# Performance work log

Hardware: AMD Instinct MI355X
Metric: run time of the kernel (lower is better)

## Reference

```python
import jax, jax.numpy as jnp
import numpy as np

H_NODE = 256
H_EDGE = 64
B = 8        # number of graphs
A_PER = 64   # anchors per graph
N_PER = 512  # nodes per graph
INF = 1000000.0
EPS = 1e-8
D_MIN, D_MAX = 0.0, 20.0  # _rbf defaults (gvp-style)


def setup_inputs() -> dict:
    key = jax.random.key(0)
    ks = jax.random.split(key, 16)
    h, he = H_NODE, H_EDGE
    n = lambda k, shp, s=1.0: jax.random.normal(k, shp, jnp.float32) * s
    return {
        "anchor_x": n(ks[0], (B * A_PER, 3), 10.0),
        "node_x": n(ks[1], (B * N_PER, 3), 10.0),
        "anchor_features": n(ks[2], (B * A_PER, h)),
        "node_features": n(ks[3], (B * N_PER, h)),
        "batch": jnp.repeat(jnp.arange(B, dtype=jnp.int32), N_PER),
        "anchor_batch": jnp.repeat(jnp.arange(B, dtype=jnp.int32), A_PER),
        "node_mask": (jax.random.uniform(ks[4], (B * N_PER,)) < 0.9).astype(jnp.float32),
        "Wq": n(ks[5], (h, h), h ** -0.5), "bq": jnp.zeros((h,), jnp.float32),
        "Wkv": n(ks[6], (2 * h, h + he), (h + he) ** -0.5), "bkv": jnp.zeros((2 * h,), jnp.float32),
        "ln1_g": jnp.ones((h,), jnp.float32), "ln1_b": jnp.zeros((h,), jnp.float32),
        "W1": n(ks[7], (2 * h, h), h ** -0.5), "b1": jnp.zeros((2 * h,), jnp.float32),
        "W2": n(ks[8], (2 * h, 2 * h), (2 * h) ** -0.5), "b2": jnp.zeros((2 * h,), jnp.float32),
        "W3": n(ks[9], (h, 2 * h), (2 * h) ** -0.5), "b3": jnp.zeros((h,), jnp.float32),
        "ln2_g": jnp.ones((h,), jnp.float32), "ln2_b": jnp.zeros((h,), jnp.float32),
    }


def _ln(x, g, b, eps=1e-5):
    m = x.mean(-1, keepdims=True)
    v = ((x - m) ** 2).mean(-1, keepdims=True)
    return (x - m) * jax.lax.rsqrt(v + eps) * g + b


def _forward(anchor_x, node_x, anchor_features, node_features, node_mask,
             Wq, bq, Wkv, bkv, ln1_g, ln1_b, W1, b1, W2, b2, W3, b3, ln2_g, ln2_b):
    h, he = H_NODE, H_EDGE
    # equal-sized graphs: reshape global tensors to [B, ., .] (batch ids are repeat(arange(B)))
    q = (anchor_features @ Wq.T + bq).reshape(B, A_PER, h)
    ax = anchor_x.reshape(B, A_PER, 3)
    nx = node_x.reshape(B, N_PER, 3)
    nf = node_features.reshape(B, N_PER, h)
    mask = node_mask.reshape(B, N_PER)

    # pairwise anchor->node distances; original adds scalar eps to the diff vector before the norm
    dist = jnp.linalg.norm(ax[:, :, None, :] - nx[:, None, :, :] + EPS, axis=-1)  # [B,A,N]

    # RBF featurization of dist/10 with D_count = h_edge
    mu = jnp.linspace(D_MIN, D_MAX, he)
    sigma = (D_MAX - D_MIN) / he
    rbf = jnp.exp(-(((dist / 10.0)[..., None] - mu) / sigma) ** 2)  # [B,A,N,he]

    # kv_node(cat([node_feat, rbf])) decomposed: node part computed once per node
    Wkv_n, Wkv_e = Wkv[:, :h], Wkv[:, h:]
    kv_n = nf @ Wkv_n.T + bkv                 # [B,N,2h]
    kv_e = rbf @ Wkv_e.T                      # [B,A,N,2h]
    kv = kv_n[:, None, :, :] + kv_e           # [B,A,N,2h]
    k, v = kv[..., :h], kv[..., h:]

    attn = jnp.einsum('bah,banh->ban', q, k)
    attn = attn * ((mask[:, None, :] - 1.0) * INF)  # faithful to original (multiplicative mask)
    attn = jax.nn.softmax(attn, axis=-1)
    upd = jnp.einsum('ban,banh->bah', attn, v).reshape(B * A_PER, h)

    af = _ln(anchor_features + upd, ln1_g, ln1_b)
    m = jax.nn.relu(af @ W1.T + b1)
    m = jax.nn.relu(m @ W2.T + b2)
    m = m @ W3.T + b3
    return _ln(af + m, ln2_g, ln2_b)


def reference(anchor_x, node_x, anchor_features, node_features, batch, anchor_batch, node_mask,
              Wq, bq, Wkv, bkv, ln1_g, ln1_b, W1, b1, W2, b2, W3, b3, ln2_g, ln2_b):
    # batch / anchor_batch encode equal-sized contiguous graphs; structure is baked into reshapes
    return _forward(anchor_x, node_x, anchor_features, node_features, node_mask,
                    Wq, bq, Wkv, bkv, ln1_g, ln1_b, W1, b1, W2, b2, W3, b3, ln2_g, ln2_b)
```

## Files before the change

kernel.cpp:

```cpp
#include <hip/hip_runtime.h>

#define H    256
#define HE   64
#define NPB  512
#define MU_STEP (20.0f / 63.0f)
#define INV_SIG 3.2f

__device__ __forceinline__ float wave_sum(float v) {
#pragma unroll
    for (int o = 32; o; o >>= 1) v += __shfl_xor(v, o, 64);
    return v;
}
__device__ __forceinline__ float wave_max(float v) {
#pragma unroll
    for (int o = 32; o; o >>= 1) v = fmaxf(v, __shfl_xor(v, o, 64));
    return v;
}
__device__ __forceinline__ float dot4(float4 a, float4 b, float acc) {
    return fmaf(a.x, b.x, fmaf(a.y, b.y, fmaf(a.z, b.z, fmaf(a.w, b.w, acc))));
}
__device__ __forceinline__ float4 add4(float4 a, float4 b) {
    return make_float4(a.x + b.x, a.y + b.y, a.z + b.z, a.w + b.w);
}

__global__ void __launch_bounds__(1024, 4) fused_all(
    const float* __restrict__ anchor_x, const float* __restrict__ node_x,
    const float* __restrict__ anchor_f, const float* __restrict__ node_f,
    const float* __restrict__ node_mask,
    const float* __restrict__ Wq,  const float* __restrict__ bq,
    const float* __restrict__ Wkv, const float* __restrict__ bkv,
    const float* __restrict__ ln1_g, const float* __restrict__ ln1_b,
    const float* __restrict__ W1, const float* __restrict__ b1,
    const float* __restrict__ W2, const float* __restrict__ b2,
    const float* __restrict__ W3, const float* __restrict__ b3,
    const float* __restrict__ g2,  const float* __restrict__ bb2,
    float* __restrict__ out)
{
    const int bid = blockIdx.x;
    const int b  = bid & 7;
    const int pr = bid >> 3;
    const int aA = b * 64 + 2 * pr;
    const int aB = aA + 1;
    const int t  = threadIdx.x;
    const int wv = t >> 6, l = t & 63;
    const int sub = l >> 4, kc16 = l & 15;

    __shared__ __align__(16) float qWp_s[2][2][324];
    __shared__ __align__(16) float q_s[2][256];
    __shared__ __align__(16) float af_s[2][256];
    __shared__ __align__(16) float d10_s[2][NPB];
    __shared__ __align__(16) float mf_s[NPB];
    __shared__ __align__(16) float lg_s[2][NPB];
    __shared__ __align__(16) float w_s[2][NPB];
    __shared__ __align__(16) float snf_s[2][256], rj_s[2][64];
    __shared__ __align__(16) float m1_s[2][512], m2_s[2][512];
    __shared__ __align__(16) float red[512], red16[32];
    __shared__ int   idx_s[2][NPB];
    __shared__ int   cnt_s[2];

    if (t < 128) {
        int hh = t >> 6, tt = t & 63;
        ((float4*)af_s[hh])[tt] =
            ((const float4*)anchor_f)[(size_t)(hh ? aB : aA) * 64 + tt];
    }
    if (t < 2) cnt_s[t] = 0;

    if (t < 512) {
        float axA0 = anchor_x[3 * aA], axA1 = anchor_x[3 * aA + 1], axA2 = anchor_x[3 * aA + 2];
        float axB0 = anchor_x[3 * aB], axB1 = anchor_x[3 * aB + 1], axB2 = anchor_x[3 * aB + 2];
        int ng = b * NPB + t;
        float nx0 = node_x[3 * ng], nx1 = node_x[3 * ng + 1], nx2 = node_x[3 * ng + 2];
        float dx = axA0 - nx0 + 1e-8f, dy = axA1 - nx1 + 1e-8f, dz = axA2 - nx2 + 1e-8f;
        d10_s[0][t] = sqrtf(dx * dx + dy * dy + dz * dz) * 0.1f;
        dx = axB0 - nx0 + 1e-8f; dy = axB1 - nx1 + 1e-8f; dz = axB2 - nx2 + 1e-8f;
        d10_s[1][t] = sqrtf(dx * dx + dy * dy + dz * dz) * 0.1f;
        mf_s[t] = (node_mask[ng] - 1.0f) * 1000000.0f;
    }
    __syncthreads();

    {
        float4 aA4[4], aB4[4];
#pragma unroll
        for (int v = 0; v < 4; ++v) {
            aA4[v] = ((const float4*)af_s[0])[16 * v + kc16];
            aB4[v] = ((const float4*)af_s[1])[16 * v + kc16];
        }
#pragma unroll
        for (int sp = 0; sp < 2; ++sp) {
            const int m0 = sp * 128 + wv * 4 + sub;
            const int m1 = m0 + 64;
            const float4* wr0 = (const float4*)(Wq + (size_t)m0 * 256);
            const float4* wr1 = (const float4*)(Wq + (size_t)m1 * 256);
            float4 w[8];
#pragma unroll
            for (int v = 0; v < 4; ++v) { w[v] = wr0[16 * v + kc16]; w[4 + v] = wr1[16 * v + kc16]; }
            float a0A = 0.f, a0B = 0.f, a1A = 0.f, a1B = 0.f;
#pragma unroll
            for (int v = 0; v < 4; ++v) {
                a0A = dot4(w[v],     aA4[v], a0A);
                a0B = dot4(w[v],     aB4[v], a0B);
                a1A = dot4(w[4 + v], aA4[v], a1A);
                a1B = dot4(w[4 + v], aB4[v], a1B);
            }
#pragma unroll
            for (int o = 8; o >= 1; o >>= 1) {
                a0A += __shfl_xor(a0A, o, 64);
                a0B += __shfl_xor(a0B, o, 64);
                a1A += __shfl_xor(a1A, o, 64);
                a1B += __shfl_xor(a1B, o, 64);
            }
            if (kc16 == 0) {
                q_s[0][m0] = a0A + bq[m0];
                q_s[1][m0] = a0B + bq[m0];
                q_s[0][m1] = a1A + bq[m1];
                q_s[1][m1] = a1B + bq[m1];
            }
        }
    }
    __syncthreads();

    {
        int grp = -1, col = 0;
        if (t < 320)                   { grp = 0; col = t; }
        else if (t >= 512 && t < 832)  { grp = 1; col = t - 512; }
        if (grp >= 0) {
            const int r0 = grp * 128;
            const float* qsA = q_s[0] + r0;
            const float* qsB = q_s[1] + r0;
            float accA = 0.f, accB = 0.f;
            for (int o = 0; o < 128; o += 16) {
                float w16[16];
#pragma unroll
                for (int u = 0; u < 16; ++u) w16[u] = Wkv[(size_t)(r0 + o + u) * 320 + col];
#pragma unroll
                for (int u = 0; u < 16; ++u) {
                    accA = fmaf(w16[u], qsA[o + u], accA);
                    accB = fmaf(w16[u], qsB[o + u], accB);
                }
            }
            qWp_s[grp][0][col] = accA;
            qWp_s[grp][1][col] = accB;
        }
    }
    {
        float p = (t < 512) ? q_s[t >> 8][t & 255] * bkv[t & 255] : 0.f;
        p = wave_sum(p);
        if (l == 0) red16[wv] = p;
    }
    __syncthreads();
    const float qbkA = red16[0] + red16[1] + red16[2] + red16[3];
    const float qbkB = red16[4] + red16[5] + red16[6] + red16[7];

    {
        const int g = sub;
        float4 qA4[4], qB4[4];
#pragma unroll
        for (int v = 0; v < 4; ++v) {
            qA4[v] = add4(((const float4*)qWp_s[0][0])[4 * kc16 + v],
                          ((const float4*)qWp_s[1][0])[4 * kc16 + v]);
            qB4[v] = add4(((const float4*)qWp_s[0][1])[4 * kc16 + v],
                          ((const float4*)qWp_s[1][1])[4 * kc16 + v]);
        }
        const float4 qeA4 = add4(((const float4*)(qWp_s[0][0] + 256))[kc16],
                                 ((const float4*)(qWp_s[1][0] + 256))[kc16]);
        const float4 qeB4 = add4(((const float4*)(qWp_s[0][1] + 256))[kc16],
                                 ((const float4*)(qWp_s[1][1] + 256))[kc16]);
        const float mu0 = (4 * kc16 + 0) * MU_STEP, mu1 = (4 * kc16 + 1) * MU_STEP;
        const float mu2 = (4 * kc16 + 2) * MU_STEP, mu3 = (4 * kc16 + 3) * MU_STEP;
        const float4* nfb = (const float4*)(node_f + (size_t)(b * NPB) * 256);

        float4 f[4], fn[4];
        {
            const size_t r0 = (size_t)(wv * 4 + g) * 64 + 4 * kc16;
#pragma unroll
            for (int v = 0; v < 4; ++v) f[v] = nfb[r0 + v];
        }
        for (int it = 0; it < 8; ++it) {
            const int n = it * 64 + wv * 4 + g;
            if (it < 7) {
                const size_t r1 = (size_t)(n + 64) * 64 + 4 * kc16;
#pragma unroll
                for (int v = 0; v < 4; ++v) fn[v] = nfb[r1 + v];
            }
            float sA = 0.f, sB = 0.f;
#pragma unroll
            for (int v = 0; v < 4; ++v) {
                sA = dot4(f[v], qA4[v], sA);
                sB = dot4(f[v], qB4[v], sB);
            }
            const float dA10 = d10_s[0][n], dB10 = d10_s[1][n];
            float u;
            u = (dA10 - mu0) * INV_SIG; sA = fmaf(qeA4.x, __expf(-u * u), sA);
            u = (dA10 - mu1) * INV_SIG; sA = fmaf(qeA4.y, __expf(-u * u), sA);
            u = (dA10 - mu2) * INV_SIG; sA = fmaf(qeA4.z, __expf(-u * u), sA);
            u = (dA10 - mu3) * INV_SIG; sA = fmaf(qeA4.w, __expf(-u * u), sA);
            u = (dB10 - mu0) * INV_SIG; sB = fmaf(qeB4.x, __expf(-u * u), sB);
            u = (dB10 - mu1) * INV_SIG; sB = fmaf(qeB4.y, __expf(-u * u), sB);
            u = (dB10 - mu2) * INV_SIG; sB = fmaf(qeB4.z, __expf(-u * u), sB);
            u = (dB10 - mu3) * INV_SIG; sB = fmaf(qeB4.w, __expf(-u * u), sB);
#pragma unroll
            for (int o = 8; o >= 1; o >>= 1) {
                sA += __shfl_xor(sA, o, 64);
                sB += __shfl_xor(sB, o, 64);
            }
            if (kc16 == 0) {
                lg_s[0][n] = (sA + qbkA) * mf_s[n];
                lg_s[1][n] = (sB + qbkB) * mf_s[n];
            }
#pragma unroll
            for (int v = 0; v < 4; ++v) f[v] = fn[v];
        }
    }
    __syncthreads();

    const int h8 = t >> 9, n9 = t & 511;
    float lg = lg_s[h8][n9];
    {
        float m = wave_max(lg);
        if (l == 0) red16[wv] = m;
    }
    __syncthreads();
    float gmA = red16[0], gmB = red16[8];
#pragma unroll
    for (int i = 1; i < 8; ++i) { gmA = fmaxf(gmA, red16[i]); gmB = fmaxf(gmB, red16[8 + i]); }
    float e = __expf(lg - (h8 ? gmB : gmA));
    w_s[h8][n9] = e;
    {
        float sm = wave_sum(e);
        if (l == 0) red16[16 + wv] = sm;
    }
    if (e > 0.f) { int p = atomicAdd(&cnt_s[h8], 1); idx_s[h8][p] = n9; }
    __syncthreads();
    float smA = 0.f, smB = 0.f;
#pragma unroll
    for (int i = 0; i < 8; ++i) { smA += red16[16 + i]; smB += red16[24 + i]; }
    const float invA = 1.0f / smA, invB = 1.0f / smB;

    if (t < 512) {
        const int hh = t >> 8, col = t & 255;
        const int cnt = cnt_s[hh];
        const float* base = node_f + (size_t)(b * NPB) * 256 + col;
        const int*   idx  = idx_s[hh];
        const float* ws   = w_s[hh];
        float s = 0.f;
        int i = 0;
        for (; i + 16 <= cnt; i += 16) {
            int   n[16];
            float f[16];
#pragma unroll
            for (int u = 0; u < 16; ++u) n[u] = idx[i + u];
#pragma unroll
            for (int u = 0; u < 16; ++u) f[u] = base[(size_t)n[u] * 256];
#pragma unroll
            for (int u = 0; u < 16; ++u) s = fmaf(ws[n[u]], f[u], s);
        }
        for (; i < cnt; ++i) { int n = idx[i]; s = fmaf(ws[n], base[(size_t)n * 256], s); }
        snf_s[hh][col] = s;
    } else {
        const int tt = t - 512;
        const int ha = tt >> 8, j = tt & 63, g = (tt >> 6) & 3;
        const int cnt = cnt_s[ha];
        const int*   idx = idx_s[ha];
        const float* ws  = w_s[ha];
        const float* ds  = d10_s[ha];
        const float mu = j * MU_STEP;
        float r = 0.f;
        int i = g;
        for (; i + 12 < cnt; i += 16) {
            int n0 = idx[i], n1 = idx[i + 4], n2 = idx[i + 8], n3 = idx[i + 12];
            float u0 = (ds[n0] - mu) * INV_SIG, u1 = (ds[n1] - mu) * INV_SIG;
            float u2 = (ds[n2] - mu) * INV_SIG, u3 = (ds[n3] - mu) * INV_SIG;
            r = fmaf(ws[n0], __expf(-u0 * u0), r);
            r = fmaf(ws[n1], __expf(-u1 * u1), r);
            r = fmaf(ws[n2], __expf(-u2 * u2), r);
            r = fmaf(ws[n3], __expf(-u3 * u3), r);
        }
        for (; i < cnt; i += 4) {
            int n = idx[i];
            float uu = (ds[n] - mu) * INV_SIG;
            r = fmaf(ws[n], __expf(-uu * uu), r);
        }
        red[tt] = r;
    }
    __syncthreads();
    if (t < 128) {
        int ha = t >> 6, j = t & 63;
        rj_s[ha][j] = red[ha * 256 + j] + red[ha * 256 + 64 + j]
                    + red[ha * 256 + 128 + j] + red[ha * 256 + 192 + j];
    }
    __syncthreads();

    {
        float4 sA4[4], sB4[4];
#pragma unroll
        for (int v = 0; v < 4; ++v) {
            sA4[v] = ((const float4*)snf_s[0])[16 * v + kc16];
            sB4[v] = ((const float4*)snf_s[1])[16 * v + kc16];
        }
        const float4 rA4 = ((const float4*)rj_s[0])[kc16];
        const float4 rB4 = ((const float4*)rj_s[1])[kc16];
#pragma unroll
        for (int pass = 0; pass < 4; ++pass) {
            int m = pass * 64 + wv * 4 + sub;
            const float4* wr = (const float4*)(Wkv + (size_t)(256 + m) * 320);
            float4 w[4];
#pragma unroll
            for (int v = 0; v < 4; ++v) w[v] = wr[16 * v + kc16];
            float4 w4 = wr[64 + kc16];
            float aAc = 0.f, aBc = 0.f;
#pragma unroll
            for (int v = 0; v < 4; ++v) {
                aAc = dot4(w[v], sA4[v], aAc);
                aBc = dot4(w[v], sB4[v], aBc);
            }
            aAc = dot4(w4, rA4, aAc);
            aBc = dot4(w4, rB4, aBc);
#pragma unroll
            for (int o = 8; o >= 1; o >>= 1) {
                aAc += __shfl_xor(aAc, o, 64);
                aBc += __shfl_xor(aBc, o, 64);
            }
            if (kc16 == 0) { red[m] = aAc; red[256 + m] = aBc; }
        }
    }
    __syncthreads();

    const int h = (t >> 8) & 1, th = t & 255;
    float x = 0.f;
    if (t < 512)
        x = af_s[h][th] + red[h * 256 + th] * (h ? invB : invA) + bkv[256 + th];
    {
        float s1 = wave_sum(x);
        float s2 = wave_sum(x * x);
        if (l == 0) { red16[wv] = s1; red16[16 + wv] = s2; }
    }
    __syncthreads();
    {
        float meanA = (red16[0] + red16[1] + red16[2] + red16[3]) * (1.0f / 256.0f);
        float meanB = (red16[4] + red16[5] + red16[6] + red16[7]) * (1.0f / 256.0f);
        float sqA   = (red16[16] + red16[17] + red16[18] + red16[19]) * (1.0f / 256.0f);
        float sqB   = (red16[20] + red16[21] + red16[22] + red16[23]) * (1.0f / 256.0f);
        float varA = sqA - meanA * meanA, varB = sqB - meanB * meanB;
        if (t < 512) {
            float xc = x - (h ? meanB : meanA);
            af_s[h][th] = xc * rsqrtf((h ? varB : varA) + 1e-5f) * ln1_g[th] + ln1_b[th];
        }
    }
    __syncthreads();

    {
        float4 aA4[4], aB4[4];
#pragma unroll
        for (int v = 0; v < 4; ++v) {
            aA4[v] = ((const float4*)af_s[0])[16 * v + kc16];
            aB4[v] = ((const float4*)af_s[1])[16 * v + kc16];
        }
#pragma unroll
        for (int sp = 0; sp < 4; ++sp) {
            const int m0 = sp * 128 + wv * 4 + sub;
            const int m1 = m0 + 64;
            const float4* wr0 = (const float4*)(W1 + (size_t)m0 * 256);
            const float4* wr1 = (const float4*)(W1 + (size_t)m1 * 256);
            float4 w[8];
#pragma unroll
            for (int v = 0; v < 4; ++v) { w[v] = wr0[16 * v + kc16]; w[4 + v] = wr1[16 * v + kc16]; }
            float a0A = 0.f, a0B = 0.f, a1A = 0.f, a1B = 0.f;
#pragma unroll
            for (int v = 0; v < 4; ++v) {
                a0A = dot4(w[v],     aA4[v], a0A);
                a0B = dot4(w[v],     aB4[v], a0B);
                a1A = dot4(w[4 + v], aA4[v], a1A);
                a1B = dot4(w[4 + v], aB4[v], a1B);
            }
#pragma unroll
            for (int o = 8; o >= 1; o >>= 1) {
                a0A += __shfl_xor(a0A, o, 64);
                a0B += __shfl_xor(a0B, o, 64);
                a1A += __shfl_xor(a1A, o, 64);
                a1B += __shfl_xor(a1B, o, 64);
            }
            if (kc16 == 0) {
                m1_s[0][m0] = fmaxf(a0A + b1[m0], 0.f);
                m1_s[1][m0] = fmaxf(a0B + b1[m0], 0.f);
                m1_s[0][m1] = fmaxf(a1A + b1[m1], 0.f);
                m1_s[1][m1] = fmaxf(a1B + b1[m1], 0.f);
            }
        }
    }
    __syncthreads();

#pragma unroll
    for (int pass = 0; pass < 8; ++pass) {
        int m = pass * 64 + wv * 4 + sub;
        const float4* wr = (const float4*)(W2 + (size_t)m * 512);
        float4 w[8];
#pragma unroll
        for (int k = 0; k < 8; ++k) w[k] = wr[k * 16 + kc16];
        const float4* mA = (const float4*)m1_s[0];
        const float4* mB = (const float4*)m1_s[1];
        float aAc = 0.f, aBc = 0.f;
#pragma unroll
        for (int k = 0; k < 8; ++k) {
            aAc = dot4(w[k], mA[k * 16 + kc16], aAc);
            aBc = dot4(w[k], mB[k * 16 + kc16], aBc);
        }
#pragma unroll
        for (int o = 8; o >= 1; o >>= 1) {
            aAc += __shfl_xor(aAc, o, 64);
            aBc += __shfl_xor(aBc, o, 64);
        }
        if (kc16 == 0) {
            float bv = b2[m];
            m2_s[0][m] = fmaxf(aAc + bv, 0.f);
            m2_s[1][m] = fmaxf(aBc + bv, 0.f);
        }
    }
    __syncthreads();

#pragma unroll
    for (int pass = 0; pass < 4; ++pass) {
        int m = pass * 64 + wv * 4 + sub;
        const float4* wr = (const float4*)(W3 + (size_t)m * 512);
        float4 w[8];
#pragma unroll
        for (int k = 0; k < 8; ++k) w[k] = wr[k * 16 + kc16];
        const float4* mA = (const float4*)m2_s[0];
        const float4* mB = (const float4*)m2_s[1];
        float aAc = 0.f, aBc = 0.f;
#pragma unroll
        for (int k = 0; k < 8; ++k) {
            aAc = dot4(w[k], mA[k * 16 + kc16], aAc);
            aBc = dot4(w[k], mB[k * 16 + kc16], aBc);
        }
#pragma unroll
        for (int o = 8; o >= 1; o >>= 1) {
            aAc += __shfl_xor(aAc, o, 64);
            aBc += __shfl_xor(aBc, o, 64);
        }
        if (kc16 == 0) {
            float bv = b3[m];
            red[m]       = aAc + bv;
            red[256 + m] = aBc + bv;
        }
    }
    __syncthreads();

    float y = 0.f;
    if (t < 512) y = red[h * 256 + th] + af_s[h][th];
    {
        float s1 = wave_sum(y);
        float s2 = wave_sum(y * y);
        if (l == 0) { red16[wv] = s1; red16[16 + wv] = s2; }
    }
    __syncthreads();
    {
        float mnA = (red16[0] + red16[1] + red16[2] + red16[3]) * (1.0f / 256.0f);
        float mnB = (red16[4] + red16[5] + red16[6] + red16[7]) * (1.0f / 256.0f);
        float sqA = (red16[16] + red16[17] + red16[18] + red16[19]) * (1.0f / 256.0f);
        float sqB = (red16[20] + red16[21] + red16[22] + red16[23]) * (1.0f / 256.0f);
        float vrA = sqA - mnA * mnA, vrB = sqB - mnB * mnB;
        if (t < 512) {
            float yc = y - (h ? mnB : mnA);
            int aOut = h ? aB : aA;
            out[(size_t)aOut * 256 + th] =
                yc * rsqrtf((h ? vrB : vrA) + 1e-5f) * g2[th] + bb2[th];
        }
    }
}

extern "C" void kernel_launch(void* const* d_in, const int* in_sizes, int n_in,
                              void* d_out, int out_size, void* d_ws, size_t ws_size,
                              hipStream_t stream)
{
    const float* anchor_x  = (const float*)d_in[0];
    const float* node_x    = (const float*)d_in[1];
    const float* anchor_f  = (const float*)d_in[2];
    const float* node_f    = (const float*)d_in[3];
    const float* node_mask = (const float*)d_in[6];
    const float* Wq        = (const float*)d_in[7];
    const float* bq        = (const float*)d_in[8];
    const float* Wkv       = (const float*)d_in[9];
    const float* bkv       = (const float*)d_in[10];
    const float* ln1_g     = (const float*)d_in[11];
    const float* ln1_b     = (const float*)d_in[12];
    const float* W1        = (const float*)d_in[13];
    const float* b1        = (const float*)d_in[14];
    const float* W2        = (const float*)d_in[15];
    const float* b2        = (const float*)d_in[16];
    const float* W3        = (const float*)d_in[17];
    const float* b3        = (const float*)d_in[18];
    const float* ln2_g     = (const float*)d_in[19];
    const float* ln2_b     = (const float*)d_in[20];

    fused_all<<<256, 1024, 0, stream>>>(anchor_x, node_x, anchor_f, node_f,
                                        node_mask, Wq, bq, Wkv, bkv,
                                        ln1_g, ln1_b, W1, b1, W2, b2, W3, b3,
                                        ln2_g, ln2_b, (float*)d_out);
}
```

Baseline: 140.3 us.

## Replace sparse index gather with dense node sweep and prefetch first weight tiles

Drops the atomic compaction of nodes with nonzero softmax weight and instead sweeps all 512 nodes densely. Each thread now accumulates both anchors over half the nodes, with a partial-sum reduction through shared memory. The RBF accumulation is also dense and uses four independent accumulators. It also prefetches the first pass of the Wq, Wkv and W1 weight rows into registers ahead of the barriers so their global latency overlaps earlier work. This removes the atomics and indirect gathers, but always reads every node's features and pays more register pressure.

```diff
diff --git a/kernel.cpp b/kernel.cpp
--- a/kernel.cpp
+++ b/kernel.cpp
@@ -52,18 +52,25 @@
     __shared__ __align__(16) float mf_s[NPB];
     __shared__ __align__(16) float lg_s[2][NPB];
     __shared__ __align__(16) float w_s[2][NPB];
+    __shared__ __align__(16) float snfp_s[2][2][256];
     __shared__ __align__(16) float snf_s[2][256], rj_s[2][64];
     __shared__ __align__(16) float m1_s[2][512], m2_s[2][512];
     __shared__ __align__(16) float red[512], red16[32];
-    __shared__ int   idx_s[2][NPB];
-    __shared__ int   cnt_s[2];
+
+    float4 wq0[8];
+    {
+        const int m0 = wv * 4 + sub;
+        const float4* wr0 = (const float4*)(Wq + (size_t)m0 * 256);
+        const float4* wr1 = (const float4*)(Wq + (size_t)(m0 + 64) * 256);
+#pragma unroll
+        for (int v = 0; v < 4; ++v) { wq0[v] = wr0[16 * v + kc16]; wq0[4 + v] = wr1[16 * v + kc16]; }
+    }
 
     if (t < 128) {
         int hh = t >> 6, tt = t & 63;
         ((float4*)af_s[hh])[tt] =
             ((const float4*)anchor_f)[(size_t)(hh ? aB : aA) * 64 + tt];
     }
-    if (t < 2) cnt_s[t] = 0;
 
     if (t < 512) {
         float axA0 = anchor_x[3 * aA], axA1 = anchor_x[3 * aA + 1], axA2 = anchor_x[3 * aA + 2];
@@ -89,11 +96,16 @@
         for (int sp = 0; sp < 2; ++sp) {
             const int m0 = sp * 128 + wv * 4 + sub;
             const int m1 = m0 + 64;
-            const float4* wr0 = (const float4*)(Wq + (size_t)m0 * 256);
-            const float4* wr1 = (const float4*)(Wq + (size_t)m1 * 256);
             float4 w[8];
-#pragma unroll
-            for (int v = 0; v < 4; ++v) { w[v] = wr0[16 * v + kc16]; w[4 + v] = wr1[16 * v + kc16]; }
+            if (sp == 0) {
+#pragma unroll
+                for (int v = 0; v < 8; ++v) w[v] = wq0[v];
+            } else {
+                const float4* wr0 = (const float4*)(Wq + (size_t)m0 * 256);
+                const float4* wr1 = (const float4*)(Wq + (size_t)m1 * 256);
+#pragma unroll
+                for (int v = 0; v < 4; ++v) { w[v] = wr0[16 * v + kc16]; w[4 + v] = wr1[16 * v + kc16]; }
+            }
             float a0A = 0.f, a0B = 0.f, a1A = 0.f, a1B = 0.f;
 #pragma unroll
             for (int v = 0; v < 4; ++v) {
@@ -229,62 +241,65 @@
         float sm = wave_sum(e);
         if (l == 0) red16[16 + wv] = sm;
     }
-    if (e > 0.f) { int p = atomicAdd(&cnt_s[h8], 1); idx_s[h8][p] = n9; }
     __syncthreads();
     float smA = 0.f, smB = 0.f;
 #pragma unroll
     for (int i = 0; i < 8; ++i) { smA += red16[16 + i]; smB += red16[24 + i]; }
     const float invA = 1.0f / smA, invB = 1.0f / smB;
 
+    float4 wu[4], wu4;
+    {
+        const float4* wr = (const float4*)(Wkv + (size_t)(256 + wv * 4 + sub) * 320);
+#pragma unroll
+        for (int v = 0; v < 4; ++v) wu[v] = wr[16 * v + kc16];
+        wu4 = wr[64 + kc16];
+    }
+
     if (t < 512) {
-        const int hh = t >> 8, col = t & 255;
-        const int cnt = cnt_s[hh];
-        const float* base = node_f + (size_t)(b * NPB) * 256 + col;
-        const int*   idx  = idx_s[hh];
-        const float* ws   = w_s[hh];
-        float s = 0.f;
-        int i = 0;
-        for (; i + 16 <= cnt; i += 16) {
-            int   n[16];
+        const int c = t & 255, seg = t >> 8;
+        const float* base = node_f + (size_t)(b * NPB + seg * 256) * 256 + c;
+        const float* wsA = w_s[0] + seg * 256;
+        const float* wsB = w_s[1] + seg * 256;
+        float sA = 0.f, sB = 0.f;
+        for (int i = 0; i < 256; i += 16) {
             float f[16];
 #pragma unroll
-            for (int u = 0; u < 16; ++u) n[u] = idx[i + u];
-#pragma unroll
-            for (int u = 0; u < 16; ++u) f[u] = base[(size_t)n[u] * 256];
-#pragma unroll
-            for (int u = 0; u < 16; ++u) s = fmaf(ws[n[u]], f[u], s);
-        }
-        for (; i < cnt; ++i) { int n = idx[i]; s = fmaf(ws[n], base[(size_t)n * 256], s); }
-        snf_s[hh][col] = s;
+            for (int u = 0; u < 16; ++u) f[u] = base[(size_t)(i + u) * 256];
+#pragma unroll
+            for (int u = 0; u < 16; ++u) {
+                sA = fmaf(wsA[i + u], f[u], sA);
+                sB = fmaf(wsB[i + u], f[u], sB);
+            }
+        }
+        snfp_s[seg][0][c] = sA;
+        snfp_s[seg][1][c] = sB;
     } else {
         const int tt = t - 512;
-        const int ha = tt >> 8, j = tt & 63, g = (tt >> 6) & 3;
-        const int cnt = cnt_s[ha];
-        const int*   idx = idx_s[ha];
-        const float* ws  = w_s[ha];
-        const float* ds  = d10_s[ha];
+        const int ha = tt >> 8, j = tt & 63, g4 = (tt >> 6) & 3;
+        const float* ws = w_s[ha];
+        const float* ds = d10_s[ha];
         const float mu = j * MU_STEP;
-        float r = 0.f;
-        int i = g;
-        for (; i + 12 < cnt; i += 16) {
-            int n0 = idx[i], n1 = idx[i + 4], n2 = idx[i + 8], n3 = idx[i + 12];
-            float u0 = (ds[n0] - mu) * INV_SIG, u1 = (ds[n1] - mu) * INV_SIG;
-            float u2 = (ds[n2] - mu) * INV_SIG, u3 = (ds[n3] - mu) * INV_SIG;
-            r = fmaf(ws[n0], __expf(-u0 * u0), r);
-            r = fmaf(ws[n1], __expf(-u1 * u1), r);
-            r = fmaf(ws[n2], __expf(-u2 * u2), r);
-            r = fmaf(ws[n3], __expf(-u3 * u3), r);
-        }
-        for (; i < cnt; i += 4) {
-            int n = idx[i];
-            float uu = (ds[n] - mu) * INV_SIG;
-            r = fmaf(ws[n], __expf(-uu * uu), r);
-        }
-        red[tt] = r;
-    }
-    __syncthreads();
-    if (t < 128) {
-        int ha = t >> 6, j = t & 63;
+        float r0 = 0.f, r1 = 0.f, r2 = 0.f, r3 = 0.f;
+        for (int i = g4; i < 512; i += 16) {
+            float u0 = (ds[i]      - mu) * INV_SIG;
+            float u1 = (ds[i + 4]  - mu) * INV_SIG;
+            float u2 = (ds[i + 8]  - mu) * INV_SIG;
+            float u3 = (ds[i + 12] - mu) * INV_SIG;
+            r0 = fmaf(ws[i],      __expf(-u0 * u0), r0);
+            r1 = fmaf(ws[i + 4],  __expf(-u1 * u1), r1);
+            r2 = fmaf(ws[i + 8],  __expf(-u2 * u2), r2);
+            r3 = fmaf(ws[i + 12], __expf(-u3 * u3), r3);
+        }
+        red[tt] = (r0 + r1) + (r2 + r3);
+    }
+    __syncthreads();
+
+    if (t < 512) {
+        const int hh = t >> 8, c = t & 255;
+        snf_s[hh][c] = snfp_s[0][hh][c] + snfp_s[1][hh][c];
+    } else if (t < 640) {
+        const int tt = t - 512;
+        int ha = tt >> 6, j = tt & 63;
         rj_s[ha][j] = red[ha * 256 + j] + red[ha * 256 + 64 + j]
                     + red[ha * 256 + 128 + j] + red[ha * 256 + 192 + j];
     }
@@ -302,11 +317,17 @@
 #pragma unroll
         for (int pass = 0; pass < 4; ++pass) {
             int m = pass * 64 + wv * 4 + sub;
-            const float4* wr = (const float4*)(Wkv + (size_t)(256 + m) * 320);
-            float4 w[4];
-#pragma unroll
-            for (int v = 0; v < 4; ++v) w[v] = wr[16 * v + kc16];
-            float4 w4 = wr[64 + kc16];
+            float4 w[4], w4;
+            if (pass == 0) {
+#pragma unroll
+                for (int v = 0; v < 4; ++v) w[v] = wu[v];
+                w4 = wu4;
+            } else {
+                const float4* wr = (const float4*)(Wkv + (size_t)(256 + m) * 320);
+#pragma unroll
+                for (int v = 0; v < 4; ++v) w[v] = wr[16 * v + kc16];
+                w4 = wr[64 + kc16];
+            }
             float aAc = 0.f, aBc = 0.f;
 #pragma unroll
             for (int v = 0; v < 4; ++v) {
@@ -324,6 +345,15 @@
         }
     }
     __syncthreads();
+
+    float4 w1p[8];
+    {
+        const int m0 = wv * 4 + sub, m1 = m0 + 64;
+        const float4* wr0 = (const float4*)(W1 + (size_t)m0 * 256);
+        const float4* wr1 = (const float4*)(W1 + (size_t)m1 * 256);
+#pragma unroll
+        for (int v = 0; v < 4; ++v) { w1p[v] = wr0[16 * v + kc16]; w1p[4 + v] = wr1[16 * v + kc16]; }
+    }
 
     const int h = (t >> 8) & 1, th = t & 255;
     float x = 0.f;
@@ -359,11 +389,16 @@
         for (int sp = 0; sp < 4; ++sp) {
             const int m0 = sp * 128 + wv * 4 + sub;
             const int m1 = m0 + 64;
-            const float4* wr0 = (const float4*)(W1 + (size_t)m0 * 256);
-            const float4* wr1 = (const float4*)(W1 + (size_t)m1 * 256);
             float4 w[8];
-#pragma unroll
-            for (int v = 0; v < 4; ++v) { w[v] = wr0[16 * v + kc16]; w[4 + v] = wr1[16 * v + kc16]; }
+            if (sp == 0) {
+#pragma unroll
+                for (int v = 0; v < 8; ++v) w[v] = w1p[v];
+            } else {
+                const float4* wr0 = (const float4*)(W1 + (size_t)m0 * 256);
+                const float4* wr1 = (const float4*)(W1 + (size_t)m1 * 256);
+#pragma unroll
+                for (int v = 0; v < 4; ++v) { w[v] = wr0[16 * v + kc16]; w[4 + v] = wr1[16 * v + kc16]; }
+            }
             float a0A = 0.f, a0B = 0.f, a1A = 0.f, a1B = 0.f;
 #pragma unroll
             for (int v = 0; v < 4; ++v) {
```

Result: slower. 145.8 us (+4.0%).
